# Kernel optimization log

Hardware: AMD Instinct MI355X
Metric: run time of the kernel (lower is better)

The kernel has to match this reference:

```python
import jax, jax.numpy as jnp
import numpy as np

NNZ = 16777216  # 2**24 nonzeros
D = 2048        # dense size (D, D, D); sum over dim 2 -> (D, D)


def setup_inputs() -> dict:
    key = jax.random.key(0)
    kv, ki = jax.random.split(key)
    values = jax.random.normal(kv, (NNZ,), dtype=jnp.float32)
    indices = jax.random.randint(ki, (3, NNZ), 0, D, dtype=jnp.int64)
    return {"values": values, "indices": indices}


def reference(values, indices):
    # sparse_coo_tensor(indices, values, size=(D,D,D)) -> sparse.sum(dim=2) -> to_dense()
    # is equivalent to a scatter-add of values keyed by (indices[0], indices[1]):
    # the third index only distinguishes entries that get summed away, and COO
    # coalescing already sums duplicate coordinates.
    out = jnp.zeros((D, D), dtype=jnp.float32)
    out = out.at[indices[0], indices[1]].add(values)
    return out
```

## Files before the change

### kernel.cpp

```cpp
#include <hip/hip_runtime.h>

#define NNZ 16777216
#define D 2048
#define NB 256
#define ROWS_PER_B 8
#define T1 512
#define EPT 32
#define CHUNK 16384
#define NCHUNK (NNZ / CHUNK)
#define SEG 17152
#define T2 1024
#define NW (T2 / 64)
#define RUNS (NCHUNK / NW)

__global__ __launch_bounds__(T1) void bin_scatter(
    const float* __restrict__ values,
    const int* __restrict__ idx0,
    const int* __restrict__ idx1,
    unsigned int* __restrict__ dump,
    unsigned int* __restrict__ pptabT)
{
    __shared__ unsigned int lhist[NB];
    __shared__ unsigned int ppref[NB];
    __shared__ unsigned int wsum[4];
    __shared__ unsigned int skey[SEG];
    __shared__ unsigned short sval[SEG];

    const int tid = threadIdx.x;
    if (tid < NB) lhist[tid] = 0;
    __syncthreads();

    const int vecBase = blockIdx.x * (CHUNK / 4);

    float4 v[8]; int4 a[8]; int4 c[8];
#pragma unroll
    for (int it = 0; it < 8; ++it) {
        int g = vecBase + it * T1 + tid;
        v[it] = reinterpret_cast<const float4*>(values)[g];
        a[it] = reinterpret_cast<const int4*>(idx0)[g];
        c[it] = reinterpret_cast<const int4*>(idx1)[g];
    }

    unsigned int outw[EPT];
    unsigned int meta[EPT];
#pragma unroll
    for (int it = 0; it < 8; ++it) {
        const int*   ap = reinterpret_cast<const int*>(&a[it]);
        const int*   cp = reinterpret_cast<const int*>(&c[it]);
        const float* vp = reinterpret_cast<const float*>(&v[it]);
#pragma unroll
        for (int e = 0; e < 4; ++e) {
            int i0 = ap[e], i1 = cp[e];
            unsigned int b = (unsigned int)i0 >> 3;
            unsigned int fb = __float_as_uint(vp[e]);
            unsigned int bf = (fb + 0x7fffu + ((fb >> 16) & 1u)) >> 16;
            outw[it * 4 + e] = ((((unsigned int)(i0 & 7) << 11) | (unsigned int)i1) << 16) | bf;
            unsigned int rk = atomicAdd(&lhist[b], 1u);
            meta[it * 4 + e] = (b << 16) | rk;
        }
    }
    __syncthreads();

    unsigned int x = 0, pc = 0, cnt = 0;
    if (tid < NB) {
        const int lane = tid & 63;
        cnt = lhist[tid];
        pc = (cnt + 3u) & ~3u;
        x = pc;
#pragma unroll
        for (int dlt = 1; dlt < 64; dlt <<= 1) {
            unsigned int y = __shfl_up(x, dlt, 64);
            if (lane >= dlt) x += y;
        }
        if (lane == 63) wsum[tid >> 6] = x;
    }
    __syncthreads();
    if (tid < NB) {
        const int wid = tid >> 6;
        unsigned int off = 0;
#pragma unroll
        for (int w = 0; w < 4; ++w) off += (w < wid) ? wsum[w] : 0u;
        unsigned int excl = x - pc + off;
        ppref[tid] = excl;
        pptabT[(size_t)tid * NCHUNK + blockIdx.x] = (excl << 16) | cnt;
    }
    __syncthreads();

#pragma unroll
    for (int e = 0; e < EPT; ++e) {
        unsigned int b  = meta[e] >> 16;
        unsigned int rk = meta[e] & 0xFFFFu;
        unsigned int slot = ppref[b] + rk;
        skey[slot] = outw[e];
        sval[slot] = 0;
    }
    __syncthreads();

    const uint4* s4 = reinterpret_cast<const uint4*>(skey);
    uint4* d4 = reinterpret_cast<uint4*>(dump + (size_t)blockIdx.x * SEG);
    for (int j = tid; j < SEG / 4; j += T1)
        d4[j] = s4[j];
}

__global__ __launch_bounds__(T2) void bucket_accumulate(
    const unsigned int* __restrict__ dump,
    const unsigned int* __restrict__ pptabT,
    float* __restrict__ out)
{
    __shared__ float tile[ROWS_PER_B * D];
    __shared__ unsigned int sdesc[NCHUNK];

    const int b = blockIdx.x;
    const int tid = threadIdx.x;
    const int w = tid >> 6;
    const int lane = tid & 63;

    for (int j = tid; j < ROWS_PER_B * D / 4; j += T2)
        reinterpret_cast<float4*>(tile)[j] = make_float4(0.f, 0.f, 0.f, 0.f);
    for (int j = tid; j < NCHUNK; j += T2)
        sdesc[j] = pptabT[(size_t)b * NCHUNK + j];
    __syncthreads();

    {
        const int nwB = T2 / 64;
        for (int j = w; j < NCHUNK; j += nwB) {
            unsigned int d = sdesc[j];
            unsigned int c = d & 0xFFFFu;
            if (c > 64u) {
                const unsigned int* base = dump + (unsigned int)j * SEG + (d >> 16);
                for (unsigned int t = 64u + (unsigned)lane; t < c; t += 64u) {
                    unsigned int ww = base[t];
                    if (ww) atomicAdd(&tile[ww >> 16], __uint_as_float(ww << 16));
                }
            }
        }
    }

    const unsigned int k0 = (unsigned int)w * RUNS;

#define PAYLOAD(kn, dsc) \
    ((lane < (int)((dsc) & 0xFFFFu)) \
        ? dump[(unsigned int)(kn) * SEG + ((dsc) >> 16) + (unsigned int)lane] : 0u)
#define ACC(wdv) if (wdv) atomicAdd(&tile[(wdv) >> 16], __uint_as_float((wdv) << 16));

    unsigned int wd0, wd1, wd2, wd3, wd4, wd5, wd6, wd7;
    {
        uint4 qa = *reinterpret_cast<const uint4*>(&sdesc[k0]);
        uint4 qb = *reinterpret_cast<const uint4*>(&sdesc[k0 + 4]);
        wd0 = PAYLOAD(k0 + 0, qa.x); wd1 = PAYLOAD(k0 + 1, qa.y);
        wd2 = PAYLOAD(k0 + 2, qa.z); wd3 = PAYLOAD(k0 + 3, qa.w);
        wd4 = PAYLOAD(k0 + 4, qb.x); wd5 = PAYLOAD(k0 + 5, qb.y);
        wd6 = PAYLOAD(k0 + 6, qb.z); wd7 = PAYLOAD(k0 + 7, qb.w);
    }

    for (int j = 0; j < RUNS - 8; j += 8) {
        uint4 na  = *reinterpret_cast<const uint4*>(&sdesc[k0 + j + 8]);
        uint4 nb_ = *reinterpret_cast<const uint4*>(&sdesc[k0 + j + 12]);
        ACC(wd0) wd0 = PAYLOAD(k0 + j + 8,  na.x);
        ACC(wd1) wd1 = PAYLOAD(k0 + j + 9,  na.y);
        ACC(wd2) wd2 = PAYLOAD(k0 + j + 10, na.z);
        ACC(wd3) wd3 = PAYLOAD(k0 + j + 11, na.w);
        ACC(wd4) wd4 = PAYLOAD(k0 + j + 12, nb_.x);
        ACC(wd5) wd5 = PAYLOAD(k0 + j + 13, nb_.y);
        ACC(wd6) wd6 = PAYLOAD(k0 + j + 14, nb_.z);
        ACC(wd7) wd7 = PAYLOAD(k0 + j + 15, nb_.w);
    }
    ACC(wd0) ACC(wd1) ACC(wd2) ACC(wd3) ACC(wd4) ACC(wd5) ACC(wd6) ACC(wd7)
#undef ACC
#undef PAYLOAD
    __syncthreads();

    float4* o4 = reinterpret_cast<float4*>(out + (size_t)b * ROWS_PER_B * D);
    for (int j = tid; j < ROWS_PER_B * D / 4; j += T2)
        o4[j] = reinterpret_cast<float4*>(tile)[j];
}

__global__ __launch_bounds__(256) void scatter_add_kernel(
    const float* __restrict__ values,
    const int* __restrict__ idx0,
    const int* __restrict__ idx1,
    float* __restrict__ out)
{
    const int nvec = NNZ / 4;
    int tid = blockIdx.x * blockDim.x + threadIdx.x;
    int stride = gridDim.x * blockDim.x;
    for (int i = tid; i < nvec; i += stride) {
        const float4 v = reinterpret_cast<const float4*>(values)[i];
        const int4   a = reinterpret_cast<const int4*>(idx0)[i];
        const int4   b = reinterpret_cast<const int4*>(idx1)[i];
        atomicAdd(&out[a.x * D + b.x], v.x);
        atomicAdd(&out[a.y * D + b.y], v.y);
        atomicAdd(&out[a.z * D + b.z], v.z);
        atomicAdd(&out[a.w * D + b.w], v.w);
    }
}

extern "C" void kernel_launch(void* const* d_in, const int* in_sizes, int n_in,
                              void* d_out, int out_size, void* d_ws, size_t ws_size,
                              hipStream_t stream) {
    const float* values  = (const float*)d_in[0];
    const int*   indices = (const int*)d_in[1];
    const int*   idx0 = indices;
    const int*   idx1 = indices + NNZ;
    float* out = (float*)d_out;

    const size_t pp_bytes = (size_t)NB * NCHUNK * sizeof(unsigned int);
    const size_t need = pp_bytes + (size_t)NCHUNK * SEG * sizeof(unsigned int);

    if (ws_size < need) {
        hipMemsetAsync(out, 0, (size_t)out_size * sizeof(float), stream);
        const int nvec = NNZ / 4;
        scatter_add_kernel<<<(nvec + 255) / 256, 256, 0, stream>>>(values, idx0, idx1, out);
        return;
    }

    unsigned int* pptabT = (unsigned int*)d_ws;
    unsigned int* dump   = (unsigned int*)((char*)d_ws + pp_bytes);

    bin_scatter<<<NCHUNK, T1, 0, stream>>>(values, idx0, idx1, dump, pptabT);
    bucket_accumulate<<<NB, T2, 0, stream>>>(dump, pptabT, out);
}
```

Baseline: 164.9 us.

## Halve chunk size and split bucket accumulation across two blocks with merge pass

Chunks shrink to 8192 elements, which doubles the number of bin_scatter blocks and makes each one lighter: fewer registers and smaller shared staging, with the unused short array removed. bucket_accumulate now runs two blocks per row bucket, each covering half of the chunks and writing to either the output or a partial buffer. A new merge kernel then adds the partial buffer into the output. This is meant to raise occupancy and parallelism on the accumulate stage (256 blocks to 512), at the cost of an extra launch and a read-modify-write of the whole 16MB output. The overflow loop also changes from lane-strided to per-thread serial.

```diff
diff --git a/kernel.cpp b/kernel.cpp
--- a/kernel.cpp
+++ b/kernel.cpp
@@ -5,13 +5,14 @@
 #define NB 256
 #define ROWS_PER_B 8
 #define T1 512
-#define EPT 32
-#define CHUNK 16384
+#define EPT 16
+#define CHUNK 8192
 #define NCHUNK (NNZ / CHUNK)
-#define SEG 17152
+#define SEG 8960
 #define T2 1024
 #define NW (T2 / 64)
-#define RUNS (NCHUNK / NW)
+#define HALF (NCHUNK / 2)
+#define RUNS (HALF / NW)
 
 __global__ __launch_bounds__(T1) void bin_scatter(
     const float* __restrict__ values,
@@ -23,8 +24,7 @@
     __shared__ unsigned int lhist[NB];
     __shared__ unsigned int ppref[NB];
     __shared__ unsigned int wsum[4];
-    __shared__ unsigned int skey[SEG];
-    __shared__ unsigned short sval[SEG];
+    __shared__ unsigned int stage[SEG];
 
     const int tid = threadIdx.x;
     if (tid < NB) lhist[tid] = 0;
@@ -32,9 +32,9 @@
 
     const int vecBase = blockIdx.x * (CHUNK / 4);
 
-    float4 v[8]; int4 a[8]; int4 c[8];
-#pragma unroll
-    for (int it = 0; it < 8; ++it) {
+    float4 v[4]; int4 a[4]; int4 c[4];
+#pragma unroll
+    for (int it = 0; it < 4; ++it) {
         int g = vecBase + it * T1 + tid;
         v[it] = reinterpret_cast<const float4*>(values)[g];
         a[it] = reinterpret_cast<const int4*>(idx0)[g];
@@ -44,7 +44,7 @@
     unsigned int outw[EPT];
     unsigned int meta[EPT];
 #pragma unroll
-    for (int it = 0; it < 8; ++it) {
+    for (int it = 0; it < 4; ++it) {
         const int*   ap = reinterpret_cast<const int*>(&a[it]);
         const int*   cp = reinterpret_cast<const int*>(&c[it]);
         const float* vp = reinterpret_cast<const float*>(&v[it]);
@@ -90,13 +90,11 @@
     for (int e = 0; e < EPT; ++e) {
         unsigned int b  = meta[e] >> 16;
         unsigned int rk = meta[e] & 0xFFFFu;
-        unsigned int slot = ppref[b] + rk;
-        skey[slot] = outw[e];
-        sval[slot] = 0;
-    }
-    __syncthreads();
-
-    const uint4* s4 = reinterpret_cast<const uint4*>(skey);
+        stage[ppref[b] + rk] = outw[e];
+    }
+    __syncthreads();
+
+    const uint4* s4 = reinterpret_cast<const uint4*>(stage);
     uint4* d4 = reinterpret_cast<uint4*>(dump + (size_t)blockIdx.x * SEG);
     for (int j = tid; j < SEG / 4; j += T1)
         d4[j] = s4[j];
@@ -105,33 +103,33 @@
 __global__ __launch_bounds__(T2) void bucket_accumulate(
     const unsigned int* __restrict__ dump,
     const unsigned int* __restrict__ pptabT,
-    float* __restrict__ out)
+    float* __restrict__ out,
+    float* __restrict__ part)
 {
     __shared__ float tile[ROWS_PER_B * D];
-    __shared__ unsigned int sdesc[NCHUNK];
-
-    const int b = blockIdx.x;
+    __shared__ unsigned int sdesc[HALF];
+
+    const int b = blockIdx.x >> 1;
+    const int h = blockIdx.x & 1;
     const int tid = threadIdx.x;
     const int w = tid >> 6;
     const int lane = tid & 63;
+    const unsigned int cbase = (unsigned int)h * HALF;
 
     for (int j = tid; j < ROWS_PER_B * D / 4; j += T2)
         reinterpret_cast<float4*>(tile)[j] = make_float4(0.f, 0.f, 0.f, 0.f);
-    for (int j = tid; j < NCHUNK; j += T2)
-        sdesc[j] = pptabT[(size_t)b * NCHUNK + j];
-    __syncthreads();
-
-    {
-        const int nwB = T2 / 64;
-        for (int j = w; j < NCHUNK; j += nwB) {
-            unsigned int d = sdesc[j];
-            unsigned int c = d & 0xFFFFu;
-            if (c > 64u) {
-                const unsigned int* base = dump + (unsigned int)j * SEG + (d >> 16);
-                for (unsigned int t = 64u + (unsigned)lane; t < c; t += 64u) {
-                    unsigned int ww = base[t];
-                    if (ww) atomicAdd(&tile[ww >> 16], __uint_as_float(ww << 16));
-                }
+    for (int j = tid; j < HALF; j += T2)
+        sdesc[j] = pptabT[(size_t)b * NCHUNK + cbase + j];
+    __syncthreads();
+
+    for (int j = tid; j < HALF; j += T2) {
+        unsigned int d = sdesc[j];
+        unsigned int c = d & 0xFFFFu;
+        if (c > 64u) {
+            const unsigned int* base = dump + (size_t)(cbase + (unsigned)j) * SEG + (d >> 16);
+            for (unsigned int t = 64u; t < c; ++t) {
+                unsigned int ww = base[t];
+                if (ww) atomicAdd(&tile[ww >> 16], __uint_as_float(ww << 16));
             }
         }
     }
@@ -140,7 +138,7 @@
 
 #define PAYLOAD(kn, dsc) \
     ((lane < (int)((dsc) & 0xFFFFu)) \
-        ? dump[(unsigned int)(kn) * SEG + ((dsc) >> 16) + (unsigned int)lane] : 0u)
+        ? dump[(size_t)(cbase + (unsigned int)(kn)) * SEG + ((dsc) >> 16) + (unsigned int)lane] : 0u)
 #define ACC(wdv) if (wdv) atomicAdd(&tile[(wdv) >> 16], __uint_as_float((wdv) << 16));
 
     unsigned int wd0, wd1, wd2, wd3, wd4, wd5, wd6, wd7;
@@ -170,9 +168,20 @@
 #undef PAYLOAD
     __syncthreads();
 
-    float4* o4 = reinterpret_cast<float4*>(out + (size_t)b * ROWS_PER_B * D);
+    float* dst = (h ? part : out) + (size_t)b * ROWS_PER_B * D;
+    float4* o4 = reinterpret_cast<float4*>(dst);
     for (int j = tid; j < ROWS_PER_B * D / 4; j += T2)
         o4[j] = reinterpret_cast<float4*>(tile)[j];
+}
+
+__global__ __launch_bounds__(256) void merge_out(
+    float* __restrict__ out, const float* __restrict__ part)
+{
+    int i = blockIdx.x * 256 + threadIdx.x;
+    float4 o = reinterpret_cast<float4*>(out)[i];
+    float4 p = reinterpret_cast<const float4*>(part)[i];
+    o.x += p.x; o.y += p.y; o.z += p.z; o.w += p.w;
+    reinterpret_cast<float4*>(out)[i] = o;
 }
 
 __global__ __launch_bounds__(256) void scatter_add_kernel(
@@ -204,8 +213,10 @@
     const int*   idx1 = indices + NNZ;
     float* out = (float*)d_out;
 
-    const size_t pp_bytes = (size_t)NB * NCHUNK * sizeof(unsigned int);
-    const size_t need = pp_bytes + (size_t)NCHUNK * SEG * sizeof(unsigned int);
+    const size_t pp_bytes   = (size_t)NB * NCHUNK * sizeof(unsigned int);
+    const size_t dump_bytes = (size_t)NCHUNK * SEG * sizeof(unsigned int);
+    const size_t part_bytes = (size_t)NB * ROWS_PER_B * D * sizeof(float);
+    const size_t need = pp_bytes + dump_bytes + part_bytes;
 
     if (ws_size < need) {
         hipMemsetAsync(out, 0, (size_t)out_size * sizeof(float), stream);
@@ -216,7 +227,9 @@
 
     unsigned int* pptabT = (unsigned int*)d_ws;
     unsigned int* dump   = (unsigned int*)((char*)d_ws + pp_bytes);
+    float*        part   = (float*)((char*)d_ws + pp_bytes + dump_bytes);
 
     bin_scatter<<<NCHUNK, T1, 0, stream>>>(values, idx0, idx1, dump, pptabT);
-    bucket_accumulate<<<NB, T2, 0, stream>>>(dump, pptabT, out);
-}
+    bucket_accumulate<<<2 * NB, T2, 0, stream>>>(dump, pptabT, out, part);
+    merge_out<<<(NB * ROWS_PER_B * D / 4) / 256, 256, 0, stream>>>(out, part);
+}
```

Measured after the change: 157.3 us. -4.6%, faster.
